# Kernel tuning notes

Measured on AMD Instinct MI355X. Metric: run time of the kernel, lower is better.

## Reference

```python
import jax, jax.numpy as jnp
import numpy as np

B, L, H, E = 4480, 7, 8, 64   # B = actual_batch * N_stations
S, D = 56, 64                 # kv length (mete features), head dim
N_STATIONS = 35
ACTUAL_B = B // N_STATIONS    # 128
NOISE_STD = 0.1
NOISE_MEAN = 0.0


def setup_inputs() -> dict:
    key = jax.random.key(0)
    k1, k2, k3, k4, k5 = jax.random.split(key, 5)
    queries = jax.random.normal(k1, (B, L, H, E), dtype=jnp.float32)
    keys = jax.random.normal(k2, (B, S, H, E), dtype=jnp.float32)
    values = jax.random.normal(k3, (B, S, H, D), dtype=jnp.float32)
    prob_matrix = jax.random.uniform(k4, (N_STATIONS, L, S), dtype=jnp.float32)
    noise = jax.random.normal(k5, (ACTUAL_B, N_STATIONS, S, H, D), dtype=jnp.float32)
    return {"queries": queries, "keys": keys, "values": values,
            "prob_matrix": prob_matrix, "noise": noise}


def reference(queries, keys, values, prob_matrix, noise):
    b, l, h, e = queries.shape
    s, d = values.shape[1], values.shape[3]
    n = prob_matrix.shape[0]
    ab = b // n  # actual batch size per station group
    scale = 1.0 / np.sqrt(e)

    # scores: [b, h, l, s]; softmax over kv axis (dropout is identity at eval)
    scores = jnp.einsum('blhe,bshe->bhls', queries, keys)
    A = jax.nn.softmax(scale * scores, axis=-1)

    # station-specific prob matrix, clamped to [0,1] as in validation
    P = jnp.clip(prob_matrix, 0.0, 1.0)[None, :, None, :, :]  # [1, n, 1, l, s]

    values_r = values.reshape(ab, n, s, h, d)
    A_r = A.reshape(ab, n, h, l, s)
    Z = noise * NOISE_STD + NOISE_MEAN  # gaussian noise, std=0.1, mean=0

    V_orig = jnp.einsum('bnhls,bnshd->bnlhd', A_r * P, values_r)
    V_noise = jnp.einsum('bnhls,bnshd->bnlhd', A_r * (1.0 - P), Z)
    V = (V_orig + V_noise).reshape(b, l, h, d)
    return V
```

## Files before the change

kernel.cpp:

```cpp
#include <hip/hip_runtime.h>
#include <math.h>


namespace {
constexpr int kL = 7;
constexpr int kH = 8;
constexpr int kE = 64;
constexpr int kS = 56;
constexpr int kD = 64;
constexpr int kN = 35;
constexpr float kScale = 0.125f;
constexpr float kNoiseStd = 0.1f;
constexpr int kWaves = 4;
}

typedef float f32x4 __attribute__((ext_vector_type(4)));
typedef float f32x2 __attribute__((ext_vector_type(2)));

__global__ __launch_bounds__(256, 2)
void fullattn_fused_kernel(const float* __restrict__ Q,
                           const float* __restrict__ K,
                           const float* __restrict__ V,
                           const float* __restrict__ P,
                           const float* __restrict__ Z,
                           float* __restrict__ O)
{
    __shared__ f32x2 sW[kWaves][kL * kS];

    const int tid  = threadIdx.x;
    const int wid  = tid >> 6;
    const int lane = tid & 63;
    const int sl   = lane >> 4;
    const int c    = lane & 15;

    const int pair = blockIdx.x * kWaves + wid;
    const int b = pair >> 3;
    const int h = pair & 7;
    const int n = b % kN;

    const float* qb = Q + ((size_t)b * kL * kH + h) * kE;
    const float* kb = K + ((size_t)b * kS * kH + h) * kE;
    const float* vb = V + ((size_t)b * kS * kH + h) * kD;
    const float* zb = Z + ((size_t)b * kS * kH + h) * kD;

    f32x4 q4[kL];
    #pragma unroll
    for (int l = 0; l < kL; ++l)
        q4[l] = *reinterpret_cast<const f32x4*>(qb + l * (kH * kE) + 4 * c);

    float x[kL];
    #pragma unroll
    for (int l = 0; l < kL; ++l) x[l] = -INFINITY;

    #pragma unroll 2
    for (int i = 0; i < kS / 4; ++i) {
        const f32x4 k4 = *reinterpret_cast<const f32x4*>(
            kb + (4 * i + sl) * (kH * kE) + 4 * c);
        #pragma unroll
        for (int l = 0; l < kL; ++l) {
            float p = q4[l].x * k4.x + q4[l].y * k4.y
                    + q4[l].z * k4.z + q4[l].w * k4.w;
            p += __shfl_xor(p, 1);
            p += __shfl_xor(p, 2);
            p += __shfl_xor(p, 4);
            p += __shfl_xor(p, 8);
            if (c == i) x[l] = p;
        }
    }

    const int s_own = 4 * c + sl;
    const float* prow = P + (size_t)n * kL * kS;
    #pragma unroll
    for (int l = 0; l < kL; ++l) {
        const float e = __expf(x[l] * kScale);
        float sum = e;
        sum += __shfl_xor(sum, 1);
        sum += __shfl_xor(sum, 2);
        sum += __shfl_xor(sum, 4);
        sum += __shfl_xor(sum, 8);
        sum += __shfl_xor(sum, 16);
        sum += __shfl_xor(sum, 32);
        const float a = e / sum;
        if (s_own < kS) {
            float p = prow[l * kS + s_own];
            p = fminf(fmaxf(p, 0.0f), 1.0f);
            f32x2 w;
            w.x = a * p;
            w.y = a * (1.0f - p) * kNoiseStd;
            sW[wid][l * kS + s_own] = w;
        }
    }

    f32x4 acc[kL];
    #pragma unroll
    for (int l = 0; l < kL; ++l) acc[l] = (f32x4)(0.0f);

    #pragma unroll 2
    for (int i = 0; i < kS / 4; ++i) {
        const int s = 4 * i + sl;
        const f32x4 v4 = *reinterpret_cast<const f32x4*>(vb + s * (kH * kD) + 4 * c);
        const f32x4 z4 = *reinterpret_cast<const f32x4*>(zb + s * (kH * kD) + 4 * c);
        #pragma unroll
        for (int l = 0; l < kL; ++l) {
            const f32x2 w = sW[wid][l * kS + s];
            acc[l] += w.x * v4 + w.y * z4;
        }
    }

    #pragma unroll
    for (int l = 0; l < kL; ++l) {
        f32x4 a = acc[l];
        a.x += __shfl_xor(a.x, 16);
        a.y += __shfl_xor(a.y, 16);
        a.z += __shfl_xor(a.z, 16);
        a.w += __shfl_xor(a.w, 16);
        a.x += __shfl_xor(a.x, 32);
        a.y += __shfl_xor(a.y, 32);
        a.z += __shfl_xor(a.z, 32);
        a.w += __shfl_xor(a.w, 32);
        if (sl == 0) {
            *reinterpret_cast<f32x4*>(
                O + (((size_t)b * kL + l) * kH + h) * kD + 4 * c) = a;
        }
    }
}

extern "C" void kernel_launch(void* const* d_in, const int* in_sizes, int n_in,
                              void* d_out, int out_size, void* d_ws, size_t ws_size,
                              hipStream_t stream) {
    const float* Q = (const float*)d_in[0];
    const float* K = (const float*)d_in[1];
    const float* V = (const float*)d_in[2];
    const float* P = (const float*)d_in[3];
    const float* Z = (const float*)d_in[4];
    float* O = (float*)d_out;

    const int pairs = 4480 * 8;
    dim3 grid(pairs / kWaves);
    fullattn_fused_kernel<<<grid, 256, 0, stream>>>(Q, K, V, P, Z, O);
}
```

Measured before the change: 321.2 us.

## Software-pipeline V/Z loads, hoist P loads, use nontemporal loads and stores

The V/Z accumulation loop becomes a manually double-buffered pipeline. The first V/Z tiles are issued before the softmax, and each iteration prefetches the next two rows while computing the current ones. The P row loads are hoisted ahead of the QK loop so their latency overlaps compute. All global loads and the output store switch to nontemporal builtins to avoid polluting the cache with streamed data. The cost is higher register pressure under launch_bounds(256,2), plus redundant prefetches on the last iteration.

Result: faster. 303.4 us (-5.5%).

```diff
diff --git a/kernel.cpp b/kernel.cpp
--- a/kernel.cpp
+++ b/kernel.cpp
@@ -16,6 +16,10 @@
 
 typedef float f32x4 __attribute__((ext_vector_type(4)));
 typedef float f32x2 __attribute__((ext_vector_type(2)));
+
+__device__ __forceinline__ f32x4 ntload4(const float* p) {
+    return __builtin_nontemporal_load(reinterpret_cast<const f32x4*>(p));
+}
 
 __global__ __launch_bounds__(256, 2)
 void fullattn_fused_kernel(const float* __restrict__ Q,
@@ -46,7 +50,15 @@
     f32x4 q4[kL];
     #pragma unroll
     for (int l = 0; l < kL; ++l)
-        q4[l] = *reinterpret_cast<const f32x4*>(qb + l * (kH * kE) + 4 * c);
+        q4[l] = ntload4(qb + l * (kH * kE) + 4 * c);
+
+    const int s_own = 4 * c + sl;
+    const int sp = (s_own < kS) ? s_own : 0;
+    const float* prow = P + (size_t)n * kL * kS;
+    float praw[kL];
+    #pragma unroll
+    for (int l = 0; l < kL; ++l)
+        praw[l] = prow[l * kS + sp];
 
     float x[kL];
     #pragma unroll
@@ -54,8 +66,7 @@
 
     #pragma unroll 2
     for (int i = 0; i < kS / 4; ++i) {
-        const f32x4 k4 = *reinterpret_cast<const f32x4*>(
-            kb + (4 * i + sl) * (kH * kE) + 4 * c);
+        const f32x4 k4 = ntload4(kb + (4 * i + sl) * (kH * kE) + 4 * c);
         #pragma unroll
         for (int l = 0; l < kL; ++l) {
             float p = q4[l].x * k4.x + q4[l].y * k4.y
@@ -68,8 +79,11 @@
         }
     }
 
-    const int s_own = 4 * c + sl;
-    const float* prow = P + (size_t)n * kL * kS;
+    f32x4 pv0 = ntload4(vb + (0 + sl) * (kH * kD) + 4 * c);
+    f32x4 pz0 = ntload4(zb + (0 + sl) * (kH * kD) + 4 * c);
+    f32x4 pv1 = ntload4(vb + (4 + sl) * (kH * kD) + 4 * c);
+    f32x4 pz1 = ntload4(zb + (4 + sl) * (kH * kD) + 4 * c);
+
     #pragma unroll
     for (int l = 0; l < kL; ++l) {
         const float e = __expf(x[l] * kScale);
@@ -82,8 +96,7 @@
         sum += __shfl_xor(sum, 32);
         const float a = e / sum;
         if (s_own < kS) {
-            float p = prow[l * kS + s_own];
-            p = fminf(fmaxf(p, 0.0f), 1.0f);
+            const float p = fminf(fmaxf(praw[l], 0.0f), 1.0f);
             f32x2 w;
             w.x = a * p;
             w.y = a * (1.0f - p) * kNoiseStd;
@@ -95,16 +108,27 @@
     #pragma unroll
     for (int l = 0; l < kL; ++l) acc[l] = (f32x4)(0.0f);
 
-    #pragma unroll 2
-    for (int i = 0; i < kS / 4; ++i) {
-        const int s = 4 * i + sl;
-        const f32x4 v4 = *reinterpret_cast<const f32x4*>(vb + s * (kH * kD) + 4 * c);
-        const f32x4 z4 = *reinterpret_cast<const f32x4*>(zb + s * (kH * kD) + 4 * c);
+    #pragma unroll 1
+    for (int i = 0; i < kS / 4; i += 2) {
+        const int ipf = (i + 2 < kS / 4) ? (i + 2) : (kS / 4 - 2);
+        const f32x4 nv0 = ntload4(vb + (4 * ipf + sl) * (kH * kD) + 4 * c);
+        const f32x4 nz0 = ntload4(zb + (4 * ipf + sl) * (kH * kD) + 4 * c);
+        const f32x4 nv1 = ntload4(vb + (4 * ipf + 4 + sl) * (kH * kD) + 4 * c);
+        const f32x4 nz1 = ntload4(zb + (4 * ipf + 4 + sl) * (kH * kD) + 4 * c);
+
+        const int s0 = 4 * i + sl;
+        const int s1 = s0 + 4;
         #pragma unroll
         for (int l = 0; l < kL; ++l) {
-            const f32x2 w = sW[wid][l * kS + s];
-            acc[l] += w.x * v4 + w.y * z4;
+            const f32x2 w = sW[wid][l * kS + s0];
+            acc[l] += w.x * pv0 + w.y * pz0;
         }
+        #pragma unroll
+        for (int l = 0; l < kL; ++l) {
+            const f32x2 w = sW[wid][l * kS + s1];
+            acc[l] += w.x * pv1 + w.y * pz1;
+        }
+        pv0 = nv0; pz0 = nz0; pv1 = nv1; pz1 = nz1;
     }
 
     #pragma unroll
@@ -119,8 +143,8 @@
         a.z += __shfl_xor(a.z, 32);
         a.w += __shfl_xor(a.w, 32);
         if (sl == 0) {
-            *reinterpret_cast<f32x4*>(
-                O + (((size_t)b * kL + l) * kH + h) * kD + 4 * c) = a;
+            __builtin_nontemporal_store(a, reinterpret_cast<f32x4*>(
+                O + (((size_t)b * kL + l) * kH + h) * kD + 4 * c));
         }
     }
 }
```
